# Kernel optimization log

Measured on AMD Instinct MI355X. Metric: run time of the kernel, lower is better.

Reference implementation:

```python
import jax, jax.numpy as jnp
import numpy as np

B, H, M, K = 4096, 1024, 4096, 8


def setup_inputs() -> dict:
    key = jax.random.key(0)
    ks = jax.random.split(key, 9)
    s = 1.0 / np.sqrt(H)
    return {
        "a": jax.random.normal(ks[0], (B, H), dtype=jnp.float32),
        "b": jax.random.normal(ks[1], (B, H), dtype=jnp.float32),
        "memory": jax.random.normal(ks[2], (M, H), dtype=jnp.float32),
        "Wa": jax.random.uniform(ks[3], (H, H), minval=-s, maxval=s, dtype=jnp.float32),
        "ba": jax.random.uniform(ks[4], (H,), minval=-s, maxval=s, dtype=jnp.float32),
        "Wb": jax.random.uniform(ks[5], (H, H), minval=-s, maxval=s, dtype=jnp.float32),
        "bb": jax.random.uniform(ks[6], (H,), minval=-s, maxval=s, dtype=jnp.float32),
        "Wc": jax.random.uniform(ks[7], (K, 1), minval=-1.0, maxval=1.0, dtype=jnp.float32),
        "bc": jax.random.uniform(ks[8], (K,), minval=-1.0, maxval=1.0, dtype=jnp.float32),
    }


def _l2_normalize(x, eps=1e-12):
    # matches F.normalize(dim=1): x / max(||x||, eps)
    n = jnp.linalg.norm(x, axis=1, keepdims=True)
    return x / jnp.maximum(n, eps)


def reference(a, b, memory, Wa, ba, Wb, bb, Wc, bc):
    ta = a @ Wa.T + ba                      # [B, H]
    tb = b @ Wb.T + bb                      # [B, H]
    cos_a = _l2_normalize(ta) @ memory.T    # [B, M] (memory NOT normalized, as in source)
    cos_b = _l2_normalize(tb) @ memory.T    # [B, M]
    weights = jax.nn.softmax(cos_a + cos_b, axis=1)
    wm = weights @ memory                   # [B, H]
    # Linear(1, k) on [B, H, 1] then permute(0,2,1): out[b,k,h] = wm[b,h]*Wc[k,0] + bc[k]
    out = wm[:, None, :] * Wc[:, 0][None, :, None] + bc[None, :, None]  # [B, K, H]
    return out
```

## Files before the change

### kernel.cpp

```cpp
#include <hip/hip_runtime.h>
#include <stdint.h>

#define BSZ 4096
#define HDIM 1024
#define MMEM 4096
#define KOUT 8

typedef __attribute__((ext_vector_type(4))) float f32x4;
typedef __attribute__((ext_vector_type(8))) short s16x8;

__device__ __forceinline__ unsigned short f2bf(float f) {
    uint32_t u = __builtin_bit_cast(uint32_t, f);
    u += 0x7FFFu + ((u >> 16) & 1u);
    return (unsigned short)(u >> 16);
}

__global__ __launch_bounds__(256) void cvt2_f32_bf16(
    const float* __restrict__ in0, const float* __restrict__ in1,
    unsigned short* __restrict__ out, int n4) {
    int i = blockIdx.x * blockDim.x + threadIdx.x;
    if (i >= n4) return;
    const float* src = blockIdx.y ? in1 : in0;
    float4 v = reinterpret_cast<const float4*>(src)[i];
    ushort4 o;
    o.x = f2bf(v.x); o.y = f2bf(v.y); o.z = f2bf(v.z); o.w = f2bf(v.w);
    reinterpret_cast<ushort4*>(out + (size_t)blockIdx.y * n4 * 4)[i] = o;
}

__global__ __launch_bounds__(256) void transpose_cvt(
    const float* __restrict__ mem, unsigned short* __restrict__ mem_bf,
    unsigned short* __restrict__ memT, int M, int H) {
    __shared__ float tile[32][33];
    const int h0 = blockIdx.x * 32, m0 = blockIdx.y * 32;
    const int tx = threadIdx.x, ty = threadIdx.y;
#pragma unroll
    for (int j = 0; j < 4; ++j) {
        int m = m0 + ty + j * 8;
        float v = mem[(size_t)m * H + h0 + tx];
        tile[ty + j * 8][tx] = v;
        mem_bf[(size_t)m * H + h0 + tx] = f2bf(v);
    }
    __syncthreads();
#pragma unroll
    for (int j = 0; j < 4; ++j) {
        int h = h0 + ty + j * 8;
        memT[(size_t)h * M + m0 + tx] = f2bf(tile[tx][ty + j * 8]);
    }
}

template <int EPI>
__global__ __launch_bounds__(256, 2) void gemm_bt(
    const unsigned short* __restrict__ A, const unsigned short* __restrict__ Bm,
    float* __restrict__ C, unsigned short* __restrict__ Ebf,
    int N, int Kdim, int nab,
    const float* __restrict__ bias, const float* __restrict__ bias1,
    size_t zA, size_t zB, size_t zC, float* __restrict__ rowsum) {
    __shared__ alignas(16) unsigned short ldsA[4096];
    __shared__ alignas(16) unsigned short ldsB[4096];

    const int tid  = threadIdx.x;
    const int lane = tid & 63;
    const int w    = tid >> 6;
    const int wm   = w >> 1, wn = w & 1;

    const int z  = blockIdx.z;
    const int ab = z % nab;
    const int ks = z / nab;
    const int KSPLIT = gridDim.z / nab;
    const int Kc = Kdim / KSPLIT;
    A  += (size_t)ab * zA + (size_t)ks * Kc;
    Bm += (size_t)ab * zB + (size_t)ks * Kc;
    C  += (size_t)ab * zC;
    const float* bi = (ab != 0 && bias1 != nullptr) ? bias1 : bias;

    const int gx  = gridDim.x;
    const int nwg = gx * gridDim.y;
    const int lid = blockIdx.y * gx + blockIdx.x;
    const int s   = (lid & 7) * (nwg >> 3) + (lid >> 3);
    const int m0 = (s / gx) * 128, n0 = (s % gx) * 128;

    const int g0 = tid >> 6;
    const int ck = (tid >> 4) & 3;
    const int rr = tid & 15;
    size_t baseA0 = (size_t)(m0 + g0 * 16 + rr) * Kdim + ck * 8;
    size_t baseA1 = baseA0 + (size_t)64 * Kdim;
    size_t baseB0 = (size_t)(n0 + g0 * 16 + rr) * Kdim + ck * 8;
    size_t baseB1 = baseB0 + (size_t)64 * Kdim;

    char* ldsAc = (char*)ldsA;
    char* ldsBc = (char*)ldsB;
    char* dA0 = ldsAc + tid * 16;
    char* dA1 = ldsAc + 4096 + tid * 16;
    char* dB0 = ldsBc + tid * 16;
    char* dB1 = ldsBc + 4096 + tid * 16;

    f32x4 acc[4][4] = {};

    const int frOff = ((lane >> 4) * 256 + (lane & 15) * 16);

    for (int ksi = 0; ksi < Kc; ksi += 32) {
        __builtin_amdgcn_global_load_lds(
            (const __attribute__((address_space(1))) void*)(A + baseA0 + ksi),
            (__attribute__((address_space(3))) void*)dA0, 16, 0, 0);
        __builtin_amdgcn_global_load_lds(
            (const __attribute__((address_space(1))) void*)(A + baseA1 + ksi),
            (__attribute__((address_space(3))) void*)dA1, 16, 0, 0);
        __builtin_amdgcn_global_load_lds(
            (const __attribute__((address_space(1))) void*)(Bm + baseB0 + ksi),
            (__attribute__((address_space(3))) void*)dB0, 16, 0, 0);
        __builtin_amdgcn_global_load_lds(
            (const __attribute__((address_space(1))) void*)(Bm + baseB1 + ksi),
            (__attribute__((address_space(3))) void*)dB1, 16, 0, 0);
        __syncthreads();

        s16x8 af[4], bfv[4];
#pragma unroll
        for (int m = 0; m < 4; ++m)
            af[m] = *(const s16x8*)(ldsAc + (wm * 4 + m) * 1024 + frOff);
#pragma unroll
        for (int n = 0; n < 4; ++n)
            bfv[n] = *(const s16x8*)(ldsBc + (wn * 4 + n) * 1024 + frOff);
#pragma unroll
        for (int m = 0; m < 4; ++m)
#pragma unroll
            for (int n = 0; n < 4; ++n)
                acc[m][n] = __builtin_amdgcn_mfma_f32_16x16x32_bf16(
                    af[m], bfv[n], acc[m][n], 0, 0, 0);
        __syncthreads();
    }

    if (EPI == 1) {
#pragma unroll
        for (int m = 0; m < 4; ++m)
#pragma unroll
            for (int n = 0; n < 4; ++n) {
                int rowb = m0 + wm * 64 + m * 16 + (lane >> 4) * 4;
                int col  = n0 + wn * 64 + n * 16 + (lane & 15);
                float bv = (ks == 0) ? bi[col] : 0.f;
#pragma unroll
                for (int r = 0; r < 4; ++r)
                    atomicAdd(&C[(size_t)(rowb + r) * N + col], acc[m][n][r] + bv);
            }
    }

    if (EPI == 3) {
#pragma unroll
        for (int m = 0; m < 4; ++m)
#pragma unroll
            for (int n = 0; n < 4; ++n)
#pragma unroll
                for (int r = 0; r < 4; ++r)
                    acc[m][n][r] = __expf(acc[m][n][r]);
#pragma unroll
        for (int m = 0; m < 4; ++m)
#pragma unroll
            for (int n = 0; n < 4; ++n) {
                int rowb = m0 + wm * 64 + m * 16 + (lane >> 4) * 4;
                int col  = n0 + wn * 64 + n * 16 + (lane & 15);
#pragma unroll
                for (int r = 0; r < 4; ++r)
                    Ebf[(size_t)(rowb + r) * N + col] = f2bf(acc[m][n][r]);
            }
#pragma unroll
        for (int m = 0; m < 4; ++m)
#pragma unroll
            for (int r = 0; r < 4; ++r) {
                float sv = (acc[m][0][r] + acc[m][1][r]) +
                           (acc[m][2][r] + acc[m][3][r]);
                sv += __shfl_xor(sv, 1);
                sv += __shfl_xor(sv, 2);
                sv += __shfl_xor(sv, 4);
                sv += __shfl_xor(sv, 8);
                if ((lane & 15) == 0) {
                    int row = m0 + wm * 64 + m * 16 + (lane >> 4) * 4 + r;
                    atomicAdd(&rowsum[row], sv);
                }
            }
    }

    if (EPI == 5) {
#pragma unroll
        for (int m = 0; m < 4; ++m)
#pragma unroll
            for (int n = 0; n < 4; ++n) {
                int rowb = m0 + wm * 64 + m * 16 + (lane >> 4) * 4;
                int col  = n0 + wn * 64 + n * 16 + (lane & 15);
#pragma unroll
                for (int r = 0; r < 4; ++r)
                    atomicAdd(&C[(size_t)(rowb + r) * N + col], acc[m][n][r]);
            }
    }
}

__global__ __launch_bounds__(256) void norm_add(
    const float* __restrict__ ta, const float* __restrict__ tb,
    unsigned short* __restrict__ u, int H) {
    const int row = blockIdx.x;
    const int tid = threadIdx.x;
    float4 va = reinterpret_cast<const float4*>(ta + (size_t)row * H)[tid];
    float4 vb = reinterpret_cast<const float4*>(tb + (size_t)row * H)[tid];
    float sa = va.x * va.x + va.y * va.y + va.z * va.z + va.w * va.w;
    float sb = vb.x * vb.x + vb.y * vb.y + vb.z * vb.z + vb.w * vb.w;
#pragma unroll
    for (int off = 32; off; off >>= 1) {
        sa += __shfl_xor(sa, off);
        sb += __shfl_xor(sb, off);
    }
    __shared__ float reda[4], redb[4];
    if ((tid & 63) == 0) { reda[tid >> 6] = sa; redb[tid >> 6] = sb; }
    __syncthreads();
    float SA = (reda[0] + reda[1]) + (reda[2] + reda[3]);
    float SB = (redb[0] + redb[1]) + (redb[2] + redb[3]);
    float ra = 1.f / fmaxf(sqrtf(SA), 1e-12f);
    float rb = 1.f / fmaxf(sqrtf(SB), 1e-12f);
    ushort4 o;
    o.x = f2bf(va.x * ra + vb.x * rb);
    o.y = f2bf(va.y * ra + vb.y * rb);
    o.z = f2bf(va.z * ra + vb.z * rb);
    o.w = f2bf(va.w * ra + vb.w * rb);
    reinterpret_cast<ushort4*>(u + (size_t)row * H)[tid] = o;
}

__global__ __launch_bounds__(256) void hub_expand(
    const float* __restrict__ wm, const float* __restrict__ rowsum,
    const float* __restrict__ Wc, const float* __restrict__ bc,
    float* __restrict__ out) {
    const int b = blockIdx.x;
    const int t = threadIdx.x;
    float rs = 1.0f / rowsum[b];
    float4 v = reinterpret_cast<const float4*>(wm)[(size_t)b * 256 + t];
    v.x *= rs; v.y *= rs; v.z *= rs; v.w *= rs;
#pragma unroll
    for (int k = 0; k < KOUT; ++k) {
        float wv = Wc[k], bv = bc[k];
        float4 o;
        o.x = v.x * wv + bv; o.y = v.y * wv + bv;
        o.z = v.z * wv + bv; o.w = v.w * wv + bv;
        reinterpret_cast<float4*>(out)[((size_t)b * KOUT + k) * 256 + t] = o;
    }
}

extern "C" void kernel_launch(void* const* d_in, const int* in_sizes, int n_in,
                              void* d_out, int out_size, void* d_ws, size_t ws_size,
                              hipStream_t stream) {
    const float* a      = (const float*)d_in[0];
    const float* b      = (const float*)d_in[1];
    const float* memory = (const float*)d_in[2];
    const float* Wa     = (const float*)d_in[3];
    const float* ba     = (const float*)d_in[4];
    const float* Wb     = (const float*)d_in[5];
    const float* bb     = (const float*)d_in[6];
    const float* Wc     = (const float*)d_in[7];
    const float* bc     = (const float*)d_in[8];
    float* out = (float*)d_out;

    const int B = BSZ, H = HDIM, M = MMEM;
    char* ws = (char*)d_ws;
    const size_t MB = 1u << 20;
    unsigned short* a_bf   = (unsigned short*)(ws + 0 * MB);
    unsigned short* Wa_bf  = (unsigned short*)(ws + 16 * MB);
    unsigned short* mem_bf = (unsigned short*)(ws + 20 * MB);
    unsigned short* memT   = (unsigned short*)(ws + 28 * MB);
    float*          ta     = (float*)(ws + 36 * MB);
    unsigned short* e_bf   = (unsigned short*)(ws + 36 * MB);
    unsigned short* u_bf   = (unsigned short*)(ws + 68 * MB);
    float*          rowsum = (float*)(ws + 76 * MB);
    float*          wm     = (float*)(ws + 80 * MB);

    hipMemsetAsync(ta, 0, (size_t)2 * B * H * sizeof(float), stream);
    hipMemsetAsync(rowsum, 0, (size_t)B * sizeof(float), stream);
    hipMemsetAsync(wm, 0, (size_t)B * H * sizeof(float), stream);

    cvt2_f32_bf16<<<dim3(B * H / 4 / 256, 2), 256, 0, stream>>>(a, b, a_bf, B * H / 4);
    cvt2_f32_bf16<<<dim3(H * H / 4 / 256, 2), 256, 0, stream>>>(Wa, Wb, Wa_bf, H * H / 4);
    transpose_cvt<<<dim3(H / 32, M / 32), dim3(32, 8), 0, stream>>>(memory, mem_bf, memT, M, H);

    gemm_bt<1><<<dim3(H / 128, B / 128, 4), 256, 0, stream>>>(
        a_bf, Wa_bf, ta, nullptr, H, H, 2, ba, bb,
        (size_t)B * H, (size_t)H * H, (size_t)B * H, nullptr);

    norm_add<<<B, 256, 0, stream>>>(ta, ta + (size_t)B * H, u_bf, H);

    gemm_bt<3><<<dim3(M / 128, B / 128, 1), 256, 0, stream>>>(
        u_bf, mem_bf, nullptr, e_bf, M, H, 1, nullptr, nullptr,
        0, 0, 0, rowsum);

    gemm_bt<5><<<dim3(H / 128, B / 128, 4), 256, 0, stream>>>(
        e_bf, memT, wm, nullptr, H, M, 1, nullptr, nullptr,
        0, 0, 0, nullptr);

    hub_expand<<<B, 256, 0, stream>>>(wm, rowsum, Wc, bc, out);
}
```

Before: 479.5 us.

## Double-buffer GEMM LDS tiles and drop split-K atomics in projection GEMM

Turns the GEMM main loop into a two-stage LDS ping-pong, where the global-to-LDS loads for the next K tile are issued before computing on the current one. Each iteration then ends with a single waitcnt plus barrier instead of two syncthreads. The projection GEMM also stops splitting K (grid z goes from 4 to 2) and writes results with plain stores plus bias instead of atomicAdd, so the memset of ta is removed. LDS use per block doubles to 32 KB, which may limit occupancy, and the projection GEMM launches fewer blocks.

```diff
diff --git a/kernel.cpp b/kernel.cpp
--- a/kernel.cpp
+++ b/kernel.cpp
@@ -55,8 +55,8 @@
     int N, int Kdim, int nab,
     const float* __restrict__ bias, const float* __restrict__ bias1,
     size_t zA, size_t zB, size_t zC, float* __restrict__ rowsum) {
-    __shared__ alignas(16) unsigned short ldsA[4096];
-    __shared__ alignas(16) unsigned short ldsB[4096];
+    __shared__ alignas(16) unsigned short ldsA[8192];
+    __shared__ alignas(16) unsigned short ldsB[8192];
 
     const int tid  = threadIdx.x;
     const int lane = tid & 63;
@@ -89,44 +89,58 @@
 
     char* ldsAc = (char*)ldsA;
     char* ldsBc = (char*)ldsB;
-    char* dA0 = ldsAc + tid * 16;
-    char* dA1 = ldsAc + 4096 + tid * 16;
-    char* dB0 = ldsBc + tid * 16;
-    char* dB1 = ldsBc + 4096 + tid * 16;
+
+    auto STAGE = [&](int bufsel, int koff) {
+        char* sA = ldsAc + bufsel * 8192;
+        char* sB = ldsBc + bufsel * 8192;
+        __builtin_amdgcn_global_load_lds(
+            (const __attribute__((address_space(1))) void*)(A + baseA0 + koff),
+            (__attribute__((address_space(3))) void*)(sA + tid * 16), 16, 0, 0);
+        __builtin_amdgcn_global_load_lds(
+            (const __attribute__((address_space(1))) void*)(A + baseA1 + koff),
+            (__attribute__((address_space(3))) void*)(sA + 4096 + tid * 16), 16, 0, 0);
+        __builtin_amdgcn_global_load_lds(
+            (const __attribute__((address_space(1))) void*)(Bm + baseB0 + koff),
+            (__attribute__((address_space(3))) void*)(sB + tid * 16), 16, 0, 0);
+        __builtin_amdgcn_global_load_lds(
+            (const __attribute__((address_space(1))) void*)(Bm + baseB1 + koff),
+            (__attribute__((address_space(3))) void*)(sB + 4096 + tid * 16), 16, 0, 0);
+    };
 
     f32x4 acc[4][4] = {};
-
     const int frOff = ((lane >> 4) * 256 + (lane & 15) * 16);
 
-    for (int ksi = 0; ksi < Kc; ksi += 32) {
-        __builtin_amdgcn_global_load_lds(
-            (const __attribute__((address_space(1))) void*)(A + baseA0 + ksi),
-            (__attribute__((address_space(3))) void*)dA0, 16, 0, 0);
-        __builtin_amdgcn_global_load_lds(
-            (const __attribute__((address_space(1))) void*)(A + baseA1 + ksi),
-            (__attribute__((address_space(3))) void*)dA1, 16, 0, 0);
-        __builtin_amdgcn_global_load_lds(
-            (const __attribute__((address_space(1))) void*)(Bm + baseB0 + ksi),
-            (__attribute__((address_space(3))) void*)dB0, 16, 0, 0);
-        __builtin_amdgcn_global_load_lds(
-            (const __attribute__((address_space(1))) void*)(Bm + baseB1 + ksi),
-            (__attribute__((address_space(3))) void*)dB1, 16, 0, 0);
-        __syncthreads();
-
+    const int nt = Kc >> 5;
+    int cur = 0;
+
+    STAGE(0, 0);
+    asm volatile("s_waitcnt vmcnt(0)" ::: "memory");
+    __builtin_amdgcn_s_barrier();
+    __builtin_amdgcn_sched_barrier(0);
+
+    for (int t = 0; t < nt; ++t) {
+        if (t + 1 < nt) STAGE(cur ^ 1, (t + 1) << 5);
+
+        const char* bA = ldsAc + cur * 8192;
+        const char* bB = ldsBc + cur * 8192;
         s16x8 af[4], bfv[4];
 #pragma unroll
         for (int m = 0; m < 4; ++m)
-            af[m] = *(const s16x8*)(ldsAc + (wm * 4 + m) * 1024 + frOff);
+            af[m] = *(const s16x8*)(bA + (wm * 4 + m) * 1024 + frOff);
 #pragma unroll
         for (int n = 0; n < 4; ++n)
-            bfv[n] = *(const s16x8*)(ldsBc + (wn * 4 + n) * 1024 + frOff);
+            bfv[n] = *(const s16x8*)(bB + (wn * 4 + n) * 1024 + frOff);
 #pragma unroll
         for (int m = 0; m < 4; ++m)
 #pragma unroll
             for (int n = 0; n < 4; ++n)
                 acc[m][n] = __builtin_amdgcn_mfma_f32_16x16x32_bf16(
                     af[m], bfv[n], acc[m][n], 0, 0, 0);
-        __syncthreads();
+
+        asm volatile("s_waitcnt vmcnt(0)" ::: "memory");
+        __builtin_amdgcn_s_barrier();
+        __builtin_amdgcn_sched_barrier(0);
+        cur ^= 1;
     }
 
     if (EPI == 1) {
@@ -136,10 +150,10 @@
             for (int n = 0; n < 4; ++n) {
                 int rowb = m0 + wm * 64 + m * 16 + (lane >> 4) * 4;
                 int col  = n0 + wn * 64 + n * 16 + (lane & 15);
-                float bv = (ks == 0) ? bi[col] : 0.f;
+                float bv = bi[col];
 #pragma unroll
                 for (int r = 0; r < 4; ++r)
-                    atomicAdd(&C[(size_t)(rowb + r) * N + col], acc[m][n][r] + bv);
+                    C[(size_t)(rowb + r) * N + col] = acc[m][n][r] + bv;
             }
     }
 
@@ -267,7 +281,6 @@
     float*          rowsum = (float*)(ws + 76 * MB);
     float*          wm     = (float*)(ws + 80 * MB);
 
-    hipMemsetAsync(ta, 0, (size_t)2 * B * H * sizeof(float), stream);
     hipMemsetAsync(rowsum, 0, (size_t)B * sizeof(float), stream);
     hipMemsetAsync(wm, 0, (size_t)B * H * sizeof(float), stream);
 
@@ -275,7 +288,7 @@
     cvt2_f32_bf16<<<dim3(H * H / 4 / 256, 2), 256, 0, stream>>>(Wa, Wb, Wa_bf, H * H / 4);
     transpose_cvt<<<dim3(H / 32, M / 32), dim3(32, 8), 0, stream>>>(memory, mem_bf, memT, M, H);
 
-    gemm_bt<1><<<dim3(H / 128, B / 128, 4), 256, 0, stream>>>(
+    gemm_bt<1><<<dim3(H / 128, B / 128, 2), 256, 0, stream>>>(
         a_bf, Wa_bf, ta, nullptr, H, H, 2, ba, bb,
         (size_t)B * H, (size_t)H * H, (size_t)B * H, nullptr);
 
```

Measured after the change: 435.3 us. 9.2% less time.
